# Kernel tuning notes

Measured on AMD Instinct MI355X. Metric: run time of the kernel, lower is better.

The kernel has to match this reference:

```python
import jax, jax.numpy as jnp
import numpy as np

# dims matching init_kwargs / input_specs
B, N, HID = 1, 200000, 256
NH, S = 8, 64
DH = HID // NH  # 32
STD = 0.02


def setup_inputs() -> dict:
    key = jax.random.key(0)
    ks = jax.random.split(key, 12)
    x = jax.random.normal(ks[0], (B, N, HID), jnp.float32)
    attn_mask = jnp.ones((B, N), jnp.float32)
    # Linear weights stored as (in, out); torch uses y = x @ W.T + b but init is random so layout is a convention.
    W_fx = jax.random.normal(ks[1], (HID, HID), jnp.float32) * STD
    b_fx = jnp.zeros((HID,), jnp.float32)
    W_x = jax.random.normal(ks[2], (HID, HID), jnp.float32) * STD
    b_x = jnp.zeros((HID,), jnp.float32)
    W_slice = jax.random.normal(ks[3], (DH, S), jnp.float32) * STD
    b_slice = jnp.zeros((S,), jnp.float32)
    W_qkv = jax.random.normal(ks[4], (DH, 3 * DH), jnp.float32) * STD  # bias=False
    W_proj = jax.random.normal(ks[5], (HID, HID), jnp.float32) * STD
    b_proj = jnp.zeros((HID,), jnp.float32)
    temperature = jnp.full((1, NH, 1, 1), 0.5, jnp.float32)
    return dict(x=x, attn_mask=attn_mask, W_fx=W_fx, b_fx=b_fx, W_x=W_x, b_x=b_x,
                W_slice=W_slice, b_slice=b_slice, W_qkv=W_qkv,
                W_proj=W_proj, b_proj=b_proj, temperature=temperature)


def reference(x, attn_mask, W_fx, b_fx, W_x, b_x, W_slice, b_slice, W_qkv, W_proj, b_proj, temperature):
    b, n, hid = x.shape
    # project and split heads: [b, h, n, c]
    fx_mid = (x @ W_fx + b_fx).reshape(b, n, NH, DH).transpose(0, 2, 1, 3)
    x_mid = (x @ W_x + b_x).reshape(b, n, NH, DH).transpose(0, 2, 1, 3)
    # slice logits [b, h, n, s], temperature-scaled softmax over slices
    slice_logits = (x_mid @ W_slice + b_slice) / temperature
    slice_weights = jax.nn.softmax(slice_logits, axis=-1)
    slice_weights = slice_weights * attn_mask[:, None, :, None]
    slice_norm = slice_weights.sum(axis=2)[..., None]  # [b, h, s, 1]
    # weighted-pool tokens into slice tokens [b, h, s, c]
    slice_tokens = jnp.einsum('bhnc,bhns->bhsc', fx_mid, slice_weights) / (slice_norm + 1e-5)
    # SDPA over the small slice axis
    q, k, v = jnp.split(slice_tokens @ W_qkv, 3, axis=-1)
    scale = 1.0 / np.sqrt(DH).astype(np.float32)
    attn = jax.nn.softmax(jnp.einsum('bhsc,bhtc->bhst', q, k) * scale, axis=-1)
    out_slice = jnp.einsum('bhst,bhtc->bhsc', attn, v)
    # scatter back to tokens [b, h, n, c] -> [b, n, hid]
    out_x = jnp.einsum('bhsc,bhns->bhnc', out_slice, slice_weights)
    out_x = out_x.transpose(0, 2, 1, 3).reshape(b, n, hid)
    out_x = out_x * attn_mask[..., None]
    out = out_x @ W_proj + b_proj
    return out * attn_mask[..., None]
```

## Files before the change

### kernel.cpp

```cpp
#include <hip/hip_runtime.h>


#define HID 256
#define NH  8
#define DH  32
#define NS  64
#define NQ  512
#define MT  32
#define TT  64
#define PSTRIDE 16896

typedef short bf16x8 __attribute__((ext_vector_type(8)));
typedef short bf16x4 __attribute__((ext_vector_type(4)));
typedef float f32x4 __attribute__((ext_vector_type(4)));

#define MFMA(a,b,c) __builtin_amdgcn_mfma_f32_16x16x32_bf16((a),(b),(c),0,0,0)

__device__ __forceinline__ f32x4 mfma16(bf16x4 a, bf16x4 b, f32x4 c) {
#if __has_builtin(__builtin_amdgcn_mfma_f32_16x16x16bf16_1k)
  return __builtin_amdgcn_mfma_f32_16x16x16bf16_1k(a, b, c, 0, 0, 0);
#elif __has_builtin(__builtin_amdgcn_mfma_f32_16x16x16_bf16)
  return __builtin_amdgcn_mfma_f32_16x16x16_bf16(a, b, c, 0, 0, 0);
#else
  f32x4 d;
  asm("v_mfma_f32_16x16x16_bf16 %0, %1, %2, %3" : "=v"(d) : "v"(a), "v"(b), "v"(c));
  return d;
#endif
}

__device__ __forceinline__ f32x4 zero4() { f32x4 z; z[0]=0.f; z[1]=0.f; z[2]=0.f; z[3]=0.f; return z; }

__device__ __forceinline__ ushort bf_rne(float f) {
  unsigned u = __float_as_uint(f);
  return (ushort)((u + 0x7FFFu + ((u >> 16) & 1u)) >> 16);
}
__device__ __forceinline__ void split2(float f, ushort& h, ushort& l) {
  h = bf_rne(f);
  float fh = __uint_as_float(((unsigned)h) << 16);
  l = bf_rne(f - fh);
}
__device__ __forceinline__ uint pack2(float f) {
  ushort h, l; split2(f, h, l);
  return ((uint)h << 16) | (uint)l;
}

__global__ __launch_bounds__(256) void k_build_wlog(
    const float* __restrict__ Wx, const float* __restrict__ bx,
    const float* __restrict__ Wsl, const float* __restrict__ bsl,
    const float* __restrict__ temp,
    ushort* __restrict__ wlh, ushort* __restrict__ wll, float* __restrict__ blog)
{
  const int q = blockIdx.x, k = threadIdx.x;
  const int h = q >> 6, s = q & 63;
  const float it = 1.0f / temp[h];
  float acc = 0.f;
#pragma unroll
  for (int c = 0; c < DH; ++c)
    acc = fmaf(Wx[k * HID + h * DH + c], Wsl[c * NS + s], acc);
  acc *= it;
  ushort hh, ll; split2(acc, hh, ll);
  wlh[q * HID + k] = hh; wll[q * HID + k] = ll;
  if (k == 0) {
    float b = bsl[s];
    for (int c = 0; c < DH; ++c) b = fmaf(bx[h * DH + c], Wsl[c * NS + s], b);
    blog[q] = b * it;
  }
}

__global__ __launch_bounds__(256) void k_build_wfxt(
    const float* __restrict__ Wfx, ushort* __restrict__ wfxth)
{
  const int c = blockIdx.x, k = threadIdx.x;
  wfxth[c * HID + k] = bf_rne(Wfx[k * HID + c]);
}

__global__ __launch_bounds__(256) void k_build_wprojt(
    const float* __restrict__ Wproj, ushort* __restrict__ wpth, ushort* __restrict__ wptl)
{
  const int hc = blockIdx.x, j = threadIdx.x;
  ushort hh, ll; split2(Wproj[hc * HID + j], hh, ll);
  wpth[j * HID + hc] = hh; wptl[j * HID + hc] = ll;
}

__global__ __launch_bounds__(512, 4) void k_pass1(
    const float* __restrict__ x, const float* __restrict__ mask,
    const ushort* __restrict__ wlogh, const float* __restrict__ blog,
    const ushort* __restrict__ wfxth, const float* __restrict__ bfx,
    float* __restrict__ partials, int Ntok, int ntiles, int ngrid)
{
  __shared__ ushort xh[MT * 264];
  __shared__ ushort wt[NQ * 40];
  __shared__ ushort fxt[HID * 40];
  __shared__ float msk[MT];

  const int t = threadIdx.x;
  const int w = t >> 6, lane = t & 63, lr = lane & 15, lg = lane >> 4;

  float blogr[4], bfxr[2];
#pragma unroll
  for (int cf = 0; cf < 4; ++cf) blogr[cf] = blog[w * 64 + cf * 16 + lr];
#pragma unroll
  for (int cf = 0; cf < 2; ++cf) bfxr[cf] = bfx[w * 32 + cf * 16 + lr];

  f32x4 pool[4][2];
#pragma unroll
  for (int sf = 0; sf < 4; ++sf) { pool[sf][0] = zero4(); pool[sf][1] = zero4(); }
  float nacc[4] = {0.f, 0.f, 0.f, 0.f};

  for (int tile = blockIdx.x; tile < ntiles; tile += ngrid) {
    const int n0 = tile * MT;
    __syncthreads();
    {
      const int tok = t >> 4, sg = (t & 15) * 16;
      float v[16];
      if (n0 + tok < Ntok) {
        const float4* src = (const float4*)(x + (size_t)(n0 + tok) * HID + sg);
#pragma unroll
        for (int i = 0; i < 4; ++i) { float4 f = src[i]; v[i*4]=f.x; v[i*4+1]=f.y; v[i*4+2]=f.z; v[i*4+3]=f.w; }
      } else {
#pragma unroll
        for (int i = 0; i < 16; ++i) v[i] = 0.f;
      }
      union { ushort u[16]; bf16x8 v8[2]; } H;
#pragma unroll
      for (int i = 0; i < 16; ++i) H.u[i] = bf_rne(v[i]);
      *reinterpret_cast<bf16x8*>(&xh[tok * 264 + sg]) = H.v8[0];
      *reinterpret_cast<bf16x8*>(&xh[tok * 264 + sg + 8]) = H.v8[1];
      if (t < MT) msk[t] = (n0 + t < Ntok) ? mask[n0 + t] : 0.f;
    }
    __syncthreads();

    f32x4 acc[2][4];
#pragma unroll
    for (int rf = 0; rf < 2; ++rf)
#pragma unroll
      for (int cf = 0; cf < 4; ++cf) acc[rf][cf] = zero4();
#pragma unroll
    for (int kk = 0; kk < HID; kk += 32) {
      bf16x8 ah0 = *reinterpret_cast<const bf16x8*>(&xh[lr * 264 + kk + lg * 8]);
      bf16x8 ah1 = *reinterpret_cast<const bf16x8*>(&xh[(16 + lr) * 264 + kk + lg * 8]);
#pragma unroll
      for (int cf = 0; cf < 4; ++cf) {
        bf16x8 bh = *reinterpret_cast<const bf16x8*>(wlogh + (size_t)(w * 64 + cf * 16 + lr) * HID + kk + lg * 8);
        acc[0][cf] = MFMA(ah0, bh, acc[0][cf]);
        acc[1][cf] = MFMA(ah1, bh, acc[1][cf]);
      }
    }
#pragma unroll
    for (int rf = 0; rf < 2; ++rf)
#pragma unroll
      for (int r = 0; r < 4; ++r) {
        float mx = -1e30f;
#pragma unroll
        for (int cf = 0; cf < 4; ++cf) { float vv = acc[rf][cf][r] + blogr[cf]; acc[rf][cf][r] = vv; mx = fmaxf(mx, vv); }
        mx = fmaxf(mx, __shfl_xor(mx, 1)); mx = fmaxf(mx, __shfl_xor(mx, 2));
        mx = fmaxf(mx, __shfl_xor(mx, 4)); mx = fmaxf(mx, __shfl_xor(mx, 8));
        float sm = 0.f;
#pragma unroll
        for (int cf = 0; cf < 4; ++cf) { float e = __expf(acc[rf][cf][r] - mx); acc[rf][cf][r] = e; sm += e; }
        sm += __shfl_xor(sm, 1); sm += __shfl_xor(sm, 2); sm += __shfl_xor(sm, 4); sm += __shfl_xor(sm, 8);
        const float sc = msk[rf * 16 + lg * 4 + r] / sm;
#pragma unroll
        for (int cf = 0; cf < 4; ++cf) acc[rf][cf][r] *= sc;
      }
#pragma unroll
    for (int rf = 0; rf < 2; ++rf)
#pragma unroll
      for (int cf = 0; cf < 4; ++cf)
#pragma unroll
        for (int r = 0; r < 4; ++r) {
          const int tok = rf * 16 + lg * 4 + r;
          const int q = w * 64 + cf * 16 + lr;
          wt[q * 40 + tok] = bf_rne(acc[rf][cf][r]);
          nacc[cf] += acc[rf][cf][r];
        }
    f32x4 fa[2][2];
    fa[0][0] = zero4(); fa[0][1] = zero4(); fa[1][0] = zero4(); fa[1][1] = zero4();
#pragma unroll
    for (int kk = 0; kk < HID; kk += 32) {
      bf16x8 ah0 = *reinterpret_cast<const bf16x8*>(&xh[lr * 264 + kk + lg * 8]);
      bf16x8 ah1 = *reinterpret_cast<const bf16x8*>(&xh[(16 + lr) * 264 + kk + lg * 8]);
#pragma unroll
      for (int cf = 0; cf < 2; ++cf) {
        bf16x8 bh = *reinterpret_cast<const bf16x8*>(wfxth + (size_t)(w * 32 + cf * 16 + lr) * HID + kk + lg * 8);
        fa[0][cf] = MFMA(ah0, bh, fa[0][cf]);
        fa[1][cf] = MFMA(ah1, bh, fa[1][cf]);
      }
    }
#pragma unroll
    for (int rf = 0; rf < 2; ++rf)
#pragma unroll
      for (int cf = 0; cf < 2; ++cf)
#pragma unroll
        for (int r = 0; r < 4; ++r) {
          const int tok = rf * 16 + lg * 4 + r;
          const int hc = w * 32 + cf * 16 + lr;
          fxt[hc * 40 + tok] = bf_rne(fa[rf][cf][r] + bfxr[cf]);
        }
    __syncthreads();
    {
      bf16x8 b0 = *reinterpret_cast<const bf16x8*>(&fxt[(w * 32 + lr) * 40 + lg * 8]);
      bf16x8 b1 = *reinterpret_cast<const bf16x8*>(&fxt[(w * 32 + 16 + lr) * 40 + lg * 8]);
#pragma unroll
      for (int sf = 0; sf < 4; ++sf) {
        bf16x8 a = *reinterpret_cast<const bf16x8*>(&wt[(w * 64 + sf * 16 + lr) * 40 + lg * 8]);
        pool[sf][0] = MFMA(a, b0, pool[sf][0]);
        pool[sf][1] = MFMA(a, b1, pool[sf][1]);
      }
    }
  }
  float* pb = partials + (size_t)blockIdx.x * PSTRIDE;
#pragma unroll
  for (int sf = 0; sf < 4; ++sf)
#pragma unroll
    for (int cp = 0; cp < 2; ++cp)
#pragma unroll
      for (int r = 0; r < 4; ++r) {
        const int s = sf * 16 + lg * 4 + r;
        const int hcl = cp * 16 + lr;
        pb[w * 2048 + s * 32 + hcl] = pool[sf][cp][r];
      }
#pragma unroll
  for (int cf = 0; cf < 4; ++cf) {
    float v = nacc[cf];
    v += __shfl_xor(v, 16); v += __shfl_xor(v, 32);
    if (lg == 0) pb[16384 + w * 64 + cf * 16 + lr] = v;
  }
}

__global__ __launch_bounds__(256) void k_reduce_norm(
    const float* __restrict__ partials, float* __restrict__ normbuf, int nb)
{
  const int p = blockIdx.x * 256 + threadIdx.x;
  float s = 0.f;
  for (int b = 0; b < nb; ++b) s += partials[(size_t)b * PSTRIDE + 16384 + p];
  normbuf[p] = s;
}

__global__ __launch_bounds__(256) void k_reduce_num(
    const float* __restrict__ partials, const float* __restrict__ normbuf,
    float* __restrict__ st, int nb)
{
  const int pidx = blockIdx.x * 256 + threadIdx.x;
  float acc = 0.f;
  for (int b = 0; b < nb; ++b) acc += partials[(size_t)b * PSTRIDE + pidx];
  st[pidx] = acc / (normbuf[pidx >> 5] + 1e-5f);
}

__global__ __launch_bounds__(64) void k_sdpa(
    const float* __restrict__ st, const float* __restrict__ Wqkv,
    uint* __restrict__ osltp)
{
  __shared__ float stt[NS][DH + 1];
  __shared__ float kt[NS][DH + 1];
  __shared__ float vt[NS][DH + 1];
  const int h = blockIdx.x, sr = threadIdx.x;
  for (int i = sr; i < NS * DH; i += 64) stt[i >> 5][i & 31] = st[(size_t)h * NS * DH + i];
  __syncthreads();
  float qr[DH];
#pragma unroll
  for (int c = 0; c < DH; ++c) {
    float aq = 0.f, ak = 0.f, av = 0.f;
#pragma unroll
    for (int i = 0; i < DH; ++i) {
      const float sv = stt[sr][i];
      aq = fmaf(sv, Wqkv[i * 96 + c], aq);
      ak = fmaf(sv, Wqkv[i * 96 + 32 + c], ak);
      av = fmaf(sv, Wqkv[i * 96 + 64 + c], av);
    }
    qr[c] = aq; kt[sr][c] = ak; vt[sr][c] = av;
  }
  __syncthreads();
  float sc[NS];
  float m = -1e30f;
  const float scale = 0.17677669529663687f;
#pragma unroll
  for (int tt = 0; tt < NS; ++tt) {
    float a = 0.f;
#pragma unroll
    for (int c = 0; c < DH; ++c) a = fmaf(qr[c], kt[tt][c], a);
    a *= scale; sc[tt] = a; m = fmaxf(m, a);
  }
  float sum = 0.f;
#pragma unroll
  for (int tt = 0; tt < NS; ++tt) { const float e = __expf(sc[tt] - m); sc[tt] = e; sum += e; }
  const float inv = 1.f / sum;
#pragma unroll
  for (int c = 0; c < DH; ++c) {
    float o = 0.f;
#pragma unroll
    for (int tt = 0; tt < NS; ++tt) o = fmaf(sc[tt], vt[tt][c], o);
    o *= inv;
    osltp[(h * DH + c) * NS + sr] = pack2(o);
  }
}

__global__ __launch_bounds__(512, 2) void k_pass3T(
    const float* __restrict__ x, const float* __restrict__ mask,
    const ushort* __restrict__ wlogh, const ushort* __restrict__ wlogl,
    const float* __restrict__ blog,
    const uint* __restrict__ osltp,
    const ushort* __restrict__ wpth, const ushort* __restrict__ wptl,
    const float* __restrict__ bproj,
    float* __restrict__ out, int Ntok, int ntiles, int ngrid)
{
  __shared__ uint smem[TT * 268];
  __shared__ float msk[TT];
  ushort* xh = (ushort*)smem;
  ushort* xl = xh + TT * 264;
  uint*   ox32 = smem;
  float*  outs = (float*)smem;

  const int t = threadIdx.x;
  const int wv = t >> 6, lane = t & 63, lr = lane & 15, lg = lane >> 4;
  const int h = wv;

  float bprr[2];
#pragma unroll
  for (int cf = 0; cf < 2; ++cf) bprr[cf] = bproj[wv * 32 + cf * 16 + lr];
  float4 blgv[4];
#pragma unroll
  for (int cf = 0; cf < 4; ++cf)
    blgv[cf] = *reinterpret_cast<const float4*>(blog + h * 64 + cf * 16 + lg * 4);

  bf16x4 oslh[2][4], osll[2][4];
#pragma unroll
  for (int cfo = 0; cfo < 2; ++cfo)
#pragma unroll
    for (int sb = 0; sb < 4; ++sb) {
      const uint4 q = *reinterpret_cast<const uint4*>(
          osltp + (size_t)(h * DH + cfo * 16 + lr) * NS + sb * 16 + lg * 4);
      union { uint u[2]; bf16x4 v; } Hc, Lc;
      Hc.u[0] = __builtin_amdgcn_perm(q.y, q.x, 0x07060302u);
      Hc.u[1] = __builtin_amdgcn_perm(q.w, q.z, 0x07060302u);
      Lc.u[0] = __builtin_amdgcn_perm(q.y, q.x, 0x05040100u);
      Lc.u[1] = __builtin_amdgcn_perm(q.w, q.z, 0x05040100u);
      oslh[cfo][sb] = Hc.v; osll[cfo][sb] = Lc.v;
    }

  for (int tile = blockIdx.x; tile < ntiles; tile += ngrid) {
    const int n0 = tile * TT;
    __syncthreads();
    {
      const int tok = t >> 3, seg = (t & 7) * 32;
      const int n = n0 + tok;
      const float* xrow = x + (size_t)n * HID + seg;
#pragma unroll
      for (int g = 0; g < 4; ++g) {
        float v[8];
        if (n < Ntok) {
          const float4* xp = (const float4*)(xrow + g * 8);
          float4 f0 = xp[0], f1 = xp[1];
          v[0]=f0.x; v[1]=f0.y; v[2]=f0.z; v[3]=f0.w;
          v[4]=f1.x; v[5]=f1.y; v[6]=f1.z; v[7]=f1.w;
        } else {
#pragma unroll
          for (int i = 0; i < 8; ++i) v[i] = 0.f;
        }
        union { ushort u[8]; bf16x8 v8; } H, L;
#pragma unroll
        for (int i = 0; i < 8; ++i) split2(v[i], H.u[i], L.u[i]);
        *reinterpret_cast<bf16x8*>(&xh[tok * 264 + seg + g * 8]) = H.v8;
        *reinterpret_cast<bf16x8*>(&xl[tok * 264 + seg + g * 8]) = L.v8;
      }
      if (t < TT) msk[t] = (n0 + t < Ntok) ? mask[n0 + t] : 0.f;
    }
    __syncthreads();

    f32x4 acc[4][4];
#pragma unroll
    for (int rf = 0; rf < 4; ++rf)
#pragma unroll
      for (int cf = 0; cf < 4; ++cf) acc[rf][cf] = zero4();
#pragma unroll
    for (int kk = 0; kk < 8; ++kk) {
      bf16x8 bx_h[4], bx_l[4];
#pragma unroll
      for (int rf = 0; rf < 4; ++rf) {
        bx_h[rf] = *reinterpret_cast<const bf16x8*>(&xh[(rf * 16 + lr) * 264 + kk * 32 + lg * 8]);
        bx_l[rf] = *reinterpret_cast<const bf16x8*>(&xl[(rf * 16 + lr) * 264 + kk * 32 + lg * 8]);
      }
#pragma unroll
      for (int cf = 0; cf < 4; ++cf) {
        const size_t bo = (size_t)(h * 64 + cf * 16 + lr) * HID + kk * 32 + lg * 8;
        bf16x8 ah = *reinterpret_cast<const bf16x8*>(wlogh + bo);
        bf16x8 al = *reinterpret_cast<const bf16x8*>(wlogl + bo);
#pragma unroll
        for (int rf = 0; rf < 4; ++rf) {
          acc[rf][cf] = MFMA(ah, bx_h[rf], acc[rf][cf]);
          acc[rf][cf] = MFMA(al, bx_h[rf], acc[rf][cf]);
          acc[rf][cf] = MFMA(ah, bx_l[rf], acc[rf][cf]);
        }
      }
    }
#pragma unroll
    for (int rf = 0; rf < 4; ++rf) {
      float mx = -1e30f;
#pragma unroll
      for (int cf = 0; cf < 4; ++cf)
#pragma unroll
        for (int r = 0; r < 4; ++r) {
          float vv = acc[rf][cf][r] + ((const float*)&blgv[cf])[r];
          acc[rf][cf][r] = vv; mx = fmaxf(mx, vv);
        }
      mx = fmaxf(mx, __shfl_xor(mx, 16)); mx = fmaxf(mx, __shfl_xor(mx, 32));
      float sm = 0.f;
#pragma unroll
      for (int cf = 0; cf < 4; ++cf)
#pragma unroll
        for (int r = 0; r < 4; ++r) { float e = __expf(acc[rf][cf][r] - mx); acc[rf][cf][r] = e; sm += e; }
      sm += __shfl_xor(sm, 16); sm += __shfl_xor(sm, 32);
      const float sc = msk[rf * 16 + lr] / sm;
#pragma unroll
      for (int cf = 0; cf < 4; ++cf)
#pragma unroll
        for (int r = 0; r < 4; ++r) acc[rf][cf][r] *= sc;
    }
    f32x4 oxacc[4][2];
#pragma unroll
    for (int rf = 0; rf < 4; ++rf) { oxacc[rf][0] = zero4(); oxacc[rf][1] = zero4(); }
#pragma unroll
    for (int rf = 0; rf < 4; ++rf) {
      uint w32[4][4];
#pragma unroll
      for (int cf = 0; cf < 4; ++cf)
#pragma unroll
        for (int r = 0; r < 4; ++r) w32[cf][r] = pack2(acc[rf][cf][r]);
#pragma unroll
      for (int sb = 0; sb < 4; ++sb) {
        union { uint u[2]; bf16x4 v; } Hc, Lc;
        Hc.u[0] = __builtin_amdgcn_perm(w32[sb][1], w32[sb][0], 0x07060302u);
        Hc.u[1] = __builtin_amdgcn_perm(w32[sb][3], w32[sb][2], 0x07060302u);
        Lc.u[0] = __builtin_amdgcn_perm(w32[sb][1], w32[sb][0], 0x05040100u);
        Lc.u[1] = __builtin_amdgcn_perm(w32[sb][3], w32[sb][2], 0x05040100u);
#pragma unroll
        for (int cfo = 0; cfo < 2; ++cfo) {
          oxacc[rf][cfo] = mfma16(Hc.v, oslh[cfo][sb], oxacc[rf][cfo]);
          oxacc[rf][cfo] = mfma16(Lc.v, oslh[cfo][sb], oxacc[rf][cfo]);
          oxacc[rf][cfo] = mfma16(Hc.v, osll[cfo][sb], oxacc[rf][cfo]);
        }
      }
    }
    __syncthreads();
#pragma unroll
    for (int rf = 0; rf < 4; ++rf)
#pragma unroll
      for (int cfo = 0; cfo < 2; ++cfo)
#pragma unroll
        for (int r = 0; r < 4; ++r) {
          const int tok = rf * 16 + lg * 4 + r;
          const int hc = h * DH + cfo * 16 + lr;
          ox32[tok * 268 + hc] = pack2(oxacc[rf][cfo][r]);
        }
    __syncthreads();
    f32x4 s2[4][2];
#pragma unroll
    for (int rf = 0; rf < 4; ++rf) { s2[rf][0] = zero4(); s2[rf][1] = zero4(); }
#pragma unroll
    for (int kk = 0; kk < 8; ++kk) {
#pragma unroll
      for (int rf = 0; rf < 4; ++rf) {
        const uint* oxp = &ox32[(rf * 16 + lr) * 268 + kk * 32 + lg * 8];
        uint4 q0 = *reinterpret_cast<const uint4*>(oxp);
        uint4 q1 = *reinterpret_cast<const uint4*>(oxp + 4);
        union { uint u[4]; bf16x8 v; } AH, AL;
        AH.u[0] = __builtin_amdgcn_perm(q0.y, q0.x, 0x07060302u);
        AH.u[1] = __builtin_amdgcn_perm(q0.w, q0.z, 0x07060302u);
        AH.u[2] = __builtin_amdgcn_perm(q1.y, q1.x, 0x07060302u);
        AH.u[3] = __builtin_amdgcn_perm(q1.w, q1.z, 0x07060302u);
        AL.u[0] = __builtin_amdgcn_perm(q0.y, q0.x, 0x05040100u);
        AL.u[1] = __builtin_amdgcn_perm(q0.w, q0.z, 0x05040100u);
        AL.u[2] = __builtin_amdgcn_perm(q1.y, q1.x, 0x05040100u);
        AL.u[3] = __builtin_amdgcn_perm(q1.w, q1.z, 0x05040100u);
#pragma unroll
        for (int cf = 0; cf < 2; ++cf) {
          const size_t bo = (size_t)(wv * 32 + cf * 16 + lr) * HID + kk * 32 + lg * 8;
          bf16x8 bh = *reinterpret_cast<const bf16x8*>(wpth + bo);
          bf16x8 bl = *reinterpret_cast<const bf16x8*>(wptl + bo);
          s2[rf][cf] = MFMA(AH.v, bh, s2[rf][cf]);
          s2[rf][cf] = MFMA(AL.v, bh, s2[rf][cf]);
          s2[rf][cf] = MFMA(AH.v, bl, s2[rf][cf]);
        }
      }
    }
    __syncthreads();
#pragma unroll
    for (int rf = 0; rf < 4; ++rf)
#pragma unroll
      for (int cf = 0; cf < 2; ++cf)
#pragma unroll
        for (int r = 0; r < 4; ++r) {
          const int tok = rf * 16 + lg * 4 + r;
          const int j = wv * 32 + cf * 16 + lr;
          const float mk = msk[tok];
          outs[tok * 268 + j] = mk * (mk * s2[rf][cf][r] + bprr[cf]);
        }
    __syncthreads();
    {
      const int tok0 = t >> 8, col = t & 255;
#pragma unroll 4
      for (int rr = 0; rr < TT / 2; ++rr) {
        const int tok = rr * 2 + tok0;
        const int n = n0 + tok;
        if (n < Ntok) out[(size_t)n * HID + col] = outs[tok * 268 + col];
      }
    }
  }
}

extern "C" void kernel_launch(void* const* d_in, const int* in_sizes, int n_in,
                              void* d_out, int out_size, void* d_ws, size_t ws_size,
                              hipStream_t stream)
{
  const float* x     = (const float*)d_in[0];
  const float* mask  = (const float*)d_in[1];
  const float* Wfx   = (const float*)d_in[2];
  const float* bfx   = (const float*)d_in[3];
  const float* Wx    = (const float*)d_in[4];
  const float* bx    = (const float*)d_in[5];
  const float* Wsl   = (const float*)d_in[6];
  const float* bsl   = (const float*)d_in[7];
  const float* Wqkv  = (const float*)d_in[8];
  const float* Wproj = (const float*)d_in[9];
  const float* bproj = (const float*)d_in[10];
  const float* temp  = (const float*)d_in[11];
  float* out = (float*)d_out;

  const int Ntok = in_sizes[0] / HID;
  const int ntiles1 = (Ntok + MT - 1) / MT;
  const int ntiles3 = (Ntok + TT - 1) / TT;

  char* ws = (char*)d_ws;
  size_t off = 0;
  ushort* wlogh = (ushort*)(ws + off); off += (size_t)NQ * HID * 2;
  ushort* wlogl = (ushort*)(ws + off); off += (size_t)NQ * HID * 2;
  float*  blog  = (float*)(ws + off);  off += NQ * 4;
  ushort* wfxth = (ushort*)(ws + off); off += (size_t)HID * HID * 2;
  ushort* wpth  = (ushort*)(ws + off); off += (size_t)HID * HID * 2;
  ushort* wptl  = (ushort*)(ws + off); off += (size_t)HID * HID * 2;
  uint*   osltp = (uint*)(ws + off);   off += (size_t)NQ * DH * 4;
  float*  stb   = (float*)(ws + off);  off += (size_t)NQ * DH * 4;
  float*  normb = (float*)(ws + off);  off += NQ * 4;
  int nb1 = 512;
  while (nb1 > 1 && off + (size_t)nb1 * PSTRIDE * 4 > ws_size) nb1 >>= 1;
  float* partials = (float*)(ws + off);

  k_build_wlog<<<dim3(NQ), dim3(256), 0, stream>>>(Wx, bx, Wsl, bsl, temp, wlogh, wlogl, blog);
  k_build_wfxt<<<dim3(HID), dim3(256), 0, stream>>>(Wfx, wfxth);
  k_build_wprojt<<<dim3(HID), dim3(256), 0, stream>>>(Wproj, wpth, wptl);
  k_pass1<<<dim3(nb1), dim3(512), 0, stream>>>(x, mask, wlogh, blog, wfxth, bfx,
                                               partials, Ntok, ntiles1, nb1);
  k_reduce_norm<<<dim3(2), dim3(256), 0, stream>>>(partials, normb, nb1);
  k_reduce_num<<<dim3(64), dim3(256), 0, stream>>>(partials, normb, stb, nb1);
  k_sdpa<<<dim3(NH), dim3(64), 0, stream>>>(stb, Wqkv, osltp);
  k_pass3T<<<dim3(256), dim3(512), 0, stream>>>(x, mask, wlogh, wlogl, blog,
                                                osltp, wpth, wptl, bproj,
                                                out, Ntok, ntiles3, 256);
}
```

Baseline: 1.371 ms.

## Keep slice weights and fx in registers for pooling MFMA in pass1

Pass1 is restructured so each wave handles one head and computes the slice-logit and fx projections together over a 64-token tile. The softmax weights and fx values are packed straight from the accumulator registers into bf16 fragments and fed into a 16x16x16 MFMA for the pooling step. This removes the shared-memory round trip through the wt/fxt staging buffers and the extra barrier. The tile grows from 32 to 64 tokens and the grid shrinks from 512 to 256 blocks, which means less partial reduction work but fewer resident blocks.

After: 1.429 ms. 1.04x slower.

```diff
diff --git a/kernel.cpp b/kernel.cpp
--- a/kernel.cpp
+++ b/kernel.cpp
@@ -6,7 +6,6 @@
 #define DH  32
 #define NS  64
 #define NQ  512
-#define MT  32
 #define TT  64
 #define PSTRIDE 16896
 
@@ -43,6 +42,11 @@
   ushort h, l; split2(f, h, l);
   return ((uint)h << 16) | (uint)l;
 }
+__device__ __forceinline__ bf16x4 pack4(float a0, float a1, float a2, float a3) {
+  union { ushort u[4]; bf16x4 v; } P;
+  P.u[0] = bf_rne(a0); P.u[1] = bf_rne(a1); P.u[2] = bf_rne(a2); P.u[3] = bf_rne(a3);
+  return P.v;
+}
 
 __global__ __launch_bounds__(256) void k_build_wlog(
     const float* __restrict__ Wx, const float* __restrict__ bx,
@@ -82,149 +86,134 @@
   wpth[j * HID + hc] = hh; wptl[j * HID + hc] = ll;
 }
 
-__global__ __launch_bounds__(512, 4) void k_pass1(
+__global__ __launch_bounds__(512, 4) void k_pass1T(
     const float* __restrict__ x, const float* __restrict__ mask,
     const ushort* __restrict__ wlogh, const float* __restrict__ blog,
     const ushort* __restrict__ wfxth, const float* __restrict__ bfx,
     float* __restrict__ partials, int Ntok, int ntiles, int ngrid)
 {
-  __shared__ ushort xh[MT * 264];
-  __shared__ ushort wt[NQ * 40];
-  __shared__ ushort fxt[HID * 40];
-  __shared__ float msk[MT];
+  __shared__ ushort xh[TT * 264];
+  __shared__ float msk[TT];
 
   const int t = threadIdx.x;
-  const int w = t >> 6, lane = t & 63, lr = lane & 15, lg = lane >> 4;
+  const int wv = t >> 6, lane = t & 63, lr = lane & 15, lg = lane >> 4;
+  const int h = wv;
 
   float blogr[4], bfxr[2];
 #pragma unroll
-  for (int cf = 0; cf < 4; ++cf) blogr[cf] = blog[w * 64 + cf * 16 + lr];
-#pragma unroll
-  for (int cf = 0; cf < 2; ++cf) bfxr[cf] = bfx[w * 32 + cf * 16 + lr];
+  for (int cf = 0; cf < 4; ++cf) blogr[cf] = blog[h * 64 + cf * 16 + lr];
+#pragma unroll
+  for (int cf2 = 0; cf2 < 2; ++cf2) bfxr[cf2] = bfx[h * 32 + cf2 * 16 + lr];
 
   f32x4 pool[4][2];
 #pragma unroll
-  for (int sf = 0; sf < 4; ++sf) { pool[sf][0] = zero4(); pool[sf][1] = zero4(); }
+  for (int cf = 0; cf < 4; ++cf) { pool[cf][0] = zero4(); pool[cf][1] = zero4(); }
   float nacc[4] = {0.f, 0.f, 0.f, 0.f};
 
   for (int tile = blockIdx.x; tile < ntiles; tile += ngrid) {
-    const int n0 = tile * MT;
+    const int n0 = tile * TT;
     __syncthreads();
     {
-      const int tok = t >> 4, sg = (t & 15) * 16;
-      float v[16];
-      if (n0 + tok < Ntok) {
-        const float4* src = (const float4*)(x + (size_t)(n0 + tok) * HID + sg);
-#pragma unroll
-        for (int i = 0; i < 4; ++i) { float4 f = src[i]; v[i*4]=f.x; v[i*4+1]=f.y; v[i*4+2]=f.z; v[i*4+3]=f.w; }
-      } else {
-#pragma unroll
-        for (int i = 0; i < 16; ++i) v[i] = 0.f;
-      }
-      union { ushort u[16]; bf16x8 v8[2]; } H;
-#pragma unroll
-      for (int i = 0; i < 16; ++i) H.u[i] = bf_rne(v[i]);
-      *reinterpret_cast<bf16x8*>(&xh[tok * 264 + sg]) = H.v8[0];
-      *reinterpret_cast<bf16x8*>(&xh[tok * 264 + sg + 8]) = H.v8[1];
-      if (t < MT) msk[t] = (n0 + t < Ntok) ? mask[n0 + t] : 0.f;
-    }
-    __syncthreads();
-
-    f32x4 acc[2][4];
-#pragma unroll
-    for (int rf = 0; rf < 2; ++rf)
-#pragma unroll
-      for (int cf = 0; cf < 4; ++cf) acc[rf][cf] = zero4();
-#pragma unroll
-    for (int kk = 0; kk < HID; kk += 32) {
-      bf16x8 ah0 = *reinterpret_cast<const bf16x8*>(&xh[lr * 264 + kk + lg * 8]);
-      bf16x8 ah1 = *reinterpret_cast<const bf16x8*>(&xh[(16 + lr) * 264 + kk + lg * 8]);
-#pragma unroll
-      for (int cf = 0; cf < 4; ++cf) {
-        bf16x8 bh = *reinterpret_cast<const bf16x8*>(wlogh + (size_t)(w * 64 + cf * 16 + lr) * HID + kk + lg * 8);
-        acc[0][cf] = MFMA(ah0, bh, acc[0][cf]);
-        acc[1][cf] = MFMA(ah1, bh, acc[1][cf]);
-      }
-    }
-#pragma unroll
-    for (int rf = 0; rf < 2; ++rf)
+      const int tok = t >> 3, seg = (t & 7) * 32;
+      const int n = n0 + tok;
+      const float* xrow = x + (size_t)n * HID + seg;
+#pragma unroll
+      for (int g = 0; g < 4; ++g) {
+        float v[8];
+        if (n < Ntok) {
+          const float4* xp = (const float4*)(xrow + g * 8);
+          float4 f0 = xp[0], f1 = xp[1];
+          v[0]=f0.x; v[1]=f0.y; v[2]=f0.z; v[3]=f0.w;
+          v[4]=f1.x; v[5]=f1.y; v[6]=f1.z; v[7]=f1.w;
+        } else {
+#pragma unroll
+          for (int i = 0; i < 8; ++i) v[i] = 0.f;
+        }
+        union { ushort u[8]; bf16x8 v8; } H;
+#pragma unroll
+        for (int i = 0; i < 8; ++i) H.u[i] = bf_rne(v[i]);
+        *reinterpret_cast<bf16x8*>(&xh[tok * 264 + seg + g * 8]) = H.v8;
+      }
+      if (t < TT) msk[t] = (n0 + t < Ntok) ? mask[n0 + t] : 0.f;
+    }
+    __syncthreads();
+
+#pragma unroll
+    for (int rfh = 0; rfh < 2; ++rfh) {
+      f32x4 acc[2][4];
+      f32x4 fa[2][2];
+#pragma unroll
+      for (int rr = 0; rr < 2; ++rr) {
+#pragma unroll
+        for (int cf = 0; cf < 4; ++cf) acc[rr][cf] = zero4();
+        fa[rr][0] = zero4(); fa[rr][1] = zero4();
+      }
+#pragma unroll
+      for (int kk = 0; kk < 8; ++kk) {
+        bf16x8 a0 = *reinterpret_cast<const bf16x8*>(&xh[((rfh * 2 + 0) * 16 + lr) * 264 + kk * 32 + lg * 8]);
+        bf16x8 a1 = *reinterpret_cast<const bf16x8*>(&xh[((rfh * 2 + 1) * 16 + lr) * 264 + kk * 32 + lg * 8]);
+#pragma unroll
+        for (int cf = 0; cf < 4; ++cf) {
+          bf16x8 bh = *reinterpret_cast<const bf16x8*>(wlogh + (size_t)(h * 64 + cf * 16 + lr) * HID + kk * 32 + lg * 8);
+          acc[0][cf] = MFMA(a0, bh, acc[0][cf]);
+          acc[1][cf] = MFMA(a1, bh, acc[1][cf]);
+        }
+#pragma unroll
+        for (int cf2 = 0; cf2 < 2; ++cf2) {
+          bf16x8 bf = *reinterpret_cast<const bf16x8*>(wfxth + (size_t)(h * 32 + cf2 * 16 + lr) * HID + kk * 32 + lg * 8);
+          fa[0][cf2] = MFMA(a0, bf, fa[0][cf2]);
+          fa[1][cf2] = MFMA(a1, bf, fa[1][cf2]);
+        }
+      }
+#pragma unroll
+      for (int rr = 0; rr < 2; ++rr) {
+        const int rf = rfh * 2 + rr;
+#pragma unroll
+        for (int r = 0; r < 4; ++r) {
+          float mx = -1e30f;
+#pragma unroll
+          for (int cf = 0; cf < 4; ++cf) { float vv = acc[rr][cf][r] + blogr[cf]; acc[rr][cf][r] = vv; mx = fmaxf(mx, vv); }
+          mx = fmaxf(mx, __shfl_xor(mx, 1)); mx = fmaxf(mx, __shfl_xor(mx, 2));
+          mx = fmaxf(mx, __shfl_xor(mx, 4)); mx = fmaxf(mx, __shfl_xor(mx, 8));
+          float sm = 0.f;
+#pragma unroll
+          for (int cf = 0; cf < 4; ++cf) { float e = __expf(acc[rr][cf][r] - mx); acc[rr][cf][r] = e; sm += e; }
+          sm += __shfl_xor(sm, 1); sm += __shfl_xor(sm, 2); sm += __shfl_xor(sm, 4); sm += __shfl_xor(sm, 8);
+          const float sc = msk[rf * 16 + lg * 4 + r] / sm;
+#pragma unroll
+          for (int cf = 0; cf < 4; ++cf) { acc[rr][cf][r] *= sc; nacc[cf] += acc[rr][cf][r]; }
+        }
+        bf16x4 bfrag[2];
+#pragma unroll
+        for (int cf2 = 0; cf2 < 2; ++cf2)
+          bfrag[cf2] = pack4(fa[rr][cf2][0] + bfxr[cf2], fa[rr][cf2][1] + bfxr[cf2],
+                             fa[rr][cf2][2] + bfxr[cf2], fa[rr][cf2][3] + bfxr[cf2]);
+#pragma unroll
+        for (int cf = 0; cf < 4; ++cf) {
+          bf16x4 aw = pack4(acc[rr][cf][0], acc[rr][cf][1], acc[rr][cf][2], acc[rr][cf][3]);
+#pragma unroll
+          for (int cf2 = 0; cf2 < 2; ++cf2)
+            pool[cf][cf2] = mfma16(aw, bfrag[cf2], pool[cf][cf2]);
+        }
+      }
+    }
+  }
+  float* pb = partials + (size_t)blockIdx.x * PSTRIDE;
+#pragma unroll
+  for (int cf = 0; cf < 4; ++cf)
+#pragma unroll
+    for (int cf2 = 0; cf2 < 2; ++cf2)
 #pragma unroll
       for (int r = 0; r < 4; ++r) {
-        float mx = -1e30f;
-#pragma unroll
-        for (int cf = 0; cf < 4; ++cf) { float vv = acc[rf][cf][r] + blogr[cf]; acc[rf][cf][r] = vv; mx = fmaxf(mx, vv); }
-        mx = fmaxf(mx, __shfl_xor(mx, 1)); mx = fmaxf(mx, __shfl_xor(mx, 2));
-        mx = fmaxf(mx, __shfl_xor(mx, 4)); mx = fmaxf(mx, __shfl_xor(mx, 8));
-        float sm = 0.f;
-#pragma unroll
-        for (int cf = 0; cf < 4; ++cf) { float e = __expf(acc[rf][cf][r] - mx); acc[rf][cf][r] = e; sm += e; }
-        sm += __shfl_xor(sm, 1); sm += __shfl_xor(sm, 2); sm += __shfl_xor(sm, 4); sm += __shfl_xor(sm, 8);
-        const float sc = msk[rf * 16 + lg * 4 + r] / sm;
-#pragma unroll
-        for (int cf = 0; cf < 4; ++cf) acc[rf][cf][r] *= sc;
-      }
-#pragma unroll
-    for (int rf = 0; rf < 2; ++rf)
-#pragma unroll
-      for (int cf = 0; cf < 4; ++cf)
-#pragma unroll
-        for (int r = 0; r < 4; ++r) {
-          const int tok = rf * 16 + lg * 4 + r;
-          const int q = w * 64 + cf * 16 + lr;
-          wt[q * 40 + tok] = bf_rne(acc[rf][cf][r]);
-          nacc[cf] += acc[rf][cf][r];
-        }
-    f32x4 fa[2][2];
-    fa[0][0] = zero4(); fa[0][1] = zero4(); fa[1][0] = zero4(); fa[1][1] = zero4();
-#pragma unroll
-    for (int kk = 0; kk < HID; kk += 32) {
-      bf16x8 ah0 = *reinterpret_cast<const bf16x8*>(&xh[lr * 264 + kk + lg * 8]);
-      bf16x8 ah1 = *reinterpret_cast<const bf16x8*>(&xh[(16 + lr) * 264 + kk + lg * 8]);
-#pragma unroll
-      for (int cf = 0; cf < 2; ++cf) {
-        bf16x8 bh = *reinterpret_cast<const bf16x8*>(wfxth + (size_t)(w * 32 + cf * 16 + lr) * HID + kk + lg * 8);
-        fa[0][cf] = MFMA(ah0, bh, fa[0][cf]);
-        fa[1][cf] = MFMA(ah1, bh, fa[1][cf]);
-      }
-    }
-#pragma unroll
-    for (int rf = 0; rf < 2; ++rf)
-#pragma unroll
-      for (int cf = 0; cf < 2; ++cf)
-#pragma unroll
-        for (int r = 0; r < 4; ++r) {
-          const int tok = rf * 16 + lg * 4 + r;
-          const int hc = w * 32 + cf * 16 + lr;
-          fxt[hc * 40 + tok] = bf_rne(fa[rf][cf][r] + bfxr[cf]);
-        }
-    __syncthreads();
-    {
-      bf16x8 b0 = *reinterpret_cast<const bf16x8*>(&fxt[(w * 32 + lr) * 40 + lg * 8]);
-      bf16x8 b1 = *reinterpret_cast<const bf16x8*>(&fxt[(w * 32 + 16 + lr) * 40 + lg * 8]);
-#pragma unroll
-      for (int sf = 0; sf < 4; ++sf) {
-        bf16x8 a = *reinterpret_cast<const bf16x8*>(&wt[(w * 64 + sf * 16 + lr) * 40 + lg * 8]);
-        pool[sf][0] = MFMA(a, b0, pool[sf][0]);
-        pool[sf][1] = MFMA(a, b1, pool[sf][1]);
-      }
-    }
-  }
-  float* pb = partials + (size_t)blockIdx.x * PSTRIDE;
-#pragma unroll
-  for (int sf = 0; sf < 4; ++sf)
-#pragma unroll
-    for (int cp = 0; cp < 2; ++cp)
-#pragma unroll
-      for (int r = 0; r < 4; ++r) {
-        const int s = sf * 16 + lg * 4 + r;
-        const int hcl = cp * 16 + lr;
-        pb[w * 2048 + s * 32 + hcl] = pool[sf][cp][r];
+        const int s = cf * 16 + lg * 4 + r;
+        const int hcl = cf2 * 16 + lr;
+        pb[h * 2048 + s * 32 + hcl] = pool[cf][cf2][r];
       }
 #pragma unroll
   for (int cf = 0; cf < 4; ++cf) {
     float v = nacc[cf];
     v += __shfl_xor(v, 16); v += __shfl_xor(v, 32);
-    if (lg == 0) pb[16384 + w * 64 + cf * 16 + lr] = v;
+    if (lg == 0) pb[16384 + h * 64 + cf * 16 + lr] = v;
   }
 }
 
@@ -527,8 +516,7 @@
   float* out = (float*)d_out;
 
   const int Ntok = in_sizes[0] / HID;
-  const int ntiles1 = (Ntok + MT - 1) / MT;
-  const int ntiles3 = (Ntok + TT - 1) / TT;
+  const int ntiles = (Ntok + TT - 1) / TT;
 
   char* ws = (char*)d_ws;
   size_t off = 0;
@@ -541,19 +529,19 @@
   uint*   osltp = (uint*)(ws + off);   off += (size_t)NQ * DH * 4;
   float*  stb   = (float*)(ws + off);  off += (size_t)NQ * DH * 4;
   float*  normb = (float*)(ws + off);  off += NQ * 4;
-  int nb1 = 512;
-  while (nb1 > 1 && off + (size_t)nb1 * PSTRIDE * 4 > ws_size) nb1 >>= 1;
+  int nbp = 256;
+  while (nbp > 1 && off + (size_t)nbp * PSTRIDE * 4 > ws_size) nbp >>= 1;
   float* partials = (float*)(ws + off);
 
   k_build_wlog<<<dim3(NQ), dim3(256), 0, stream>>>(Wx, bx, Wsl, bsl, temp, wlogh, wlogl, blog);
   k_build_wfxt<<<dim3(HID), dim3(256), 0, stream>>>(Wfx, wfxth);
   k_build_wprojt<<<dim3(HID), dim3(256), 0, stream>>>(Wproj, wpth, wptl);
-  k_pass1<<<dim3(nb1), dim3(512), 0, stream>>>(x, mask, wlogh, blog, wfxth, bfx,
-                                               partials, Ntok, ntiles1, nb1);
-  k_reduce_norm<<<dim3(2), dim3(256), 0, stream>>>(partials, normb, nb1);
-  k_reduce_num<<<dim3(64), dim3(256), 0, stream>>>(partials, normb, stb, nb1);
+  k_pass1T<<<dim3(nbp), dim3(512), 0, stream>>>(x, mask, wlogh, blog, wfxth, bfx,
+                                                partials, Ntok, ntiles, nbp);
+  k_reduce_norm<<<dim3(2), dim3(256), 0, stream>>>(partials, normb, nbp);
+  k_reduce_num<<<dim3(64), dim3(256), 0, stream>>>(partials, normb, stb, nbp);
   k_sdpa<<<dim3(NH), dim3(64), 0, stream>>>(stb, Wqkv, osltp);
   k_pass3T<<<dim3(256), dim3(512), 0, stream>>>(x, mask, wlogh, wlogl, blog,
                                                 osltp, wpth, wptl, bproj,
-                                                out, Ntok, ntiles3, 256);
-}
+                                                out, Ntok, ntiles, 256);
+}
```
